# Performance work log

Hardware: AMD Instinct MI355X
Metric: run time of the kernel (lower is better)

## Reference

```python
import math
import jax, jax.numpy as jnp
import numpy as np

# ---- static config (mirrors init_kwargs) ----
NLAT_I, NLON_I = 240, 480      # input equiangular grid (incl. both poles)
NLAT_O, NLON_O = 361, 720      # output equiangular grid (incl. both poles)
CI, CO = 32, 32
NR, NPHI = 3, 3                # kernel_shape
K = (NR - 1) * NPHI + 1        # anisotropic piecewise-linear DISCO basis size = 7
LMAX = 120
CUTOFF = (NR + 0.25) * math.pi / LMAX     # _compute_cutoff_radius
DLAT_O = math.pi / (NLAT_O - 1)
WOFF = int(math.ceil(CUTOFF / DLAT_O))    # half lat-window (=10); geodesic dist >= |dtheta| so window is exact
WLAT = 2 * WOFF + 1
TWO_PI = 2.0 * math.pi


def _bilinear_upsample(x):
    # ResampleS2(mode='bilinear'): x [B,C,NLAT_I,NLON_I] -> [B,C,NLAT_O,NLON_O]
    # equiangular colatitudes theta_j = pi*j/(nlat-1); periodic longitude.
    pos_t = jnp.linspace(0.0, math.pi, NLAT_O) / (math.pi / (NLAT_I - 1))
    i0 = jnp.clip(jnp.floor(pos_t).astype(jnp.int32), 0, NLAT_I - 1)
    i1 = jnp.minimum(i0 + 1, NLAT_I - 1)
    wt = (pos_t - i0).astype(x.dtype)
    xl = (1.0 - wt)[:, None] * x[:, :, i0, :] + wt[:, None] * x[:, :, i1, :]
    pos_p = (jnp.arange(NLON_O) * (TWO_PI / NLON_O)) / (TWO_PI / NLON_I)
    j0f = jnp.floor(pos_p)
    j0 = j0f.astype(jnp.int32) % NLON_I
    j1 = (j0 + 1) % NLON_I
    wp = (pos_p - j0f).astype(x.dtype)
    return (1.0 - wp) * xl[..., j0] + wp * xl[..., j1]


def _build_psi():
    # DISCO filter tensor psi[k, t_out, dlat, dlon] with quadrature merged in,
    # exploiting longitude translation invariance (computed at lon_out = 0).
    theta = jnp.linspace(0.0, math.pi, NLAT_O)
    t_idx = jnp.arange(NLAT_O)
    d_idx = jnp.arange(WLAT) - WOFF
    lat_in = t_idx[:, None] + d_idx[None, :]             # [T,W]
    valid = (lat_in >= 0) & (lat_in < NLAT_O)
    lat_in_c = jnp.clip(lat_in, 0, NLAT_O - 1)
    alpha = -theta[:, None, None]                         # [T,1,1]
    gamma = theta[lat_in_c][:, :, None]                   # [T,W,1]
    beta = (TWO_PI / NLON_O) * jnp.arange(NLON_O)[None, None, :]
    # rotate input point into frame where the output point is at the north pole
    z = jnp.cos(alpha) * jnp.cos(gamma) - jnp.cos(beta) * jnp.sin(alpha) * jnp.sin(gamma)
    xx = jnp.cos(alpha) * jnp.cos(beta) * jnp.sin(gamma) + jnp.sin(alpha) * jnp.cos(gamma)
    yy = jnp.sin(beta) * jnp.sin(gamma)
    r = jnp.arccos(jnp.clip(z, -1.0, 1.0))                # geodesic distance [T,W,P]
    phi = jnp.arctan2(yy, xx) % TWO_PI                    # local azimuth
    dr = CUTOFF / NR
    dph = TWO_PI / NPHI
    vals = [jnp.maximum(0.0, 1.0 - r / dr)]               # isotropic center hat
    for k in range(1, K):
        ir = (k - 1) // NPHI + 1
        ip = (k - 1) % NPHI
        rad = jnp.maximum(0.0, 1.0 - jnp.abs(r - ir * dr) / dr)
        dd = jnp.abs(phi - ip * dph)
        dd = jnp.minimum(dd, TWO_PI - dd)
        az = jnp.maximum(0.0, 1.0 - dd / dph)
        vals.append(rad * az)
    psi = jnp.stack(vals, 0)                              # [K,T,W,P]
    psi = psi * (r <= CUTOFF) * valid[None, :, :, None]
    # merge quadrature weights of the input grid (sin(theta) dtheta dphi)
    q = jnp.sin(theta) * (math.pi / (NLAT_O - 1)) * (TWO_PI / NLON_O)
    psi = psi * q[lat_in_c][None, :, :, None]
    # nodal L1 normalization per basis function and output node
    scale = jnp.sum(psi, axis=(2, 3), keepdims=True)
    psi = psi / jnp.maximum(scale, 1e-8)
    return psi.astype(jnp.float32), lat_in_c


def _disco_conv(xu, weight, psi, lat_in_c):
    # xu [B,Ci,T,P]; weight [Co,Ci,K]; psi [K,T,W,P]
    h = jnp.einsum('oik,bitp->boktp', weight, xu)         # fold channel mixing first
    Hh = jnp.fft.rfft(h, axis=-1)                         # [B,Co,K,T,F]
    Ph = jnp.conj(jnp.fft.rfft(psi, axis=-1))             # [K,T,W,F]
    yh = jnp.zeros(Hh.shape[:2] + (NLAT_O, Hh.shape[-1]), dtype=Hh.dtype)
    for d in range(WLAT):                                 # small fixed halo loop
        Hd = Hh[:, :, :, lat_in_c[:, d], :]               # [B,Co,K,T,F]
        yh = yh + jnp.einsum('boktf,ktf->botf', Hd, Ph[:, :, d, :])
    return jnp.fft.irfft(yh, n=NLON_O, axis=-1)           # circular correlation over lon


def setup_inputs() -> dict:
    key = jax.random.key(0)
    k1, k2 = jax.random.split(key)
    x = jax.random.normal(k1, (1, CI, NLAT_I, NLON_I), dtype=jnp.float32)
    weight = jax.random.normal(k2, (CO, CI, K), dtype=jnp.float32) * 0.05
    return {'x': x, 'weight': weight}


def reference(x, weight):
    psi, lat_in_c = _build_psi()
    xu = _bilinear_upsample(x.astype(jnp.float32))        # forced fp32 region
    y = _disco_conv(xu, weight.astype(jnp.float32), psi, lat_in_c)
    return y.astype(x.dtype)
```

## Files before the change

kernel.cpp:

```cpp
#include <hip/hip_runtime.h>
#include <hip/hip_bf16.h>
#include <math.h>

#define NLAT_I 240
#define NLON_I 480
#define NLAT_O 361
#define NLON_O 720
#define CI_N 32
#define CO_N 32
#define K_N 7
#define WOFF 10
#define WLAT 21

#define PI_F 3.14159265358979323846f
#define TWOPI_F 6.28318530717958647692f
#define DLAT_V (PI_F / 360.0f)
#define DPHI_V (TWOPI_F / 720.0f)
#define CUTOFF_V (3.25f * PI_F / 120.0f)
#define DR_V (CUTOFF_V / 3.0f)
#define IDR_V (1.0f / DR_V)
#define DPH_V (TWOPI_F / 3.0f)
#define IDPH_V (1.0f / DPH_V)
#define QF_V (DLAT_V * DPHI_V)

#define PAD_T 64
#define CT 64
#define NBLK 512
#define NC45 45
#define NE 7581

typedef __attribute__((ext_vector_type(8))) short short8v;
typedef __attribute__((ext_vector_type(4))) short short4v;
typedef __attribute__((ext_vector_type(16))) float f32x16;

__device__ __forceinline__ unsigned short f2bf(float f) {
  __hip_bfloat16 h = __float2bfloat16(f);
  union { __hip_bfloat16 b; unsigned short s; } u; u.b = h; return u.s;
}

__device__ __forceinline__ void psi_eval(float ct, float st, float cg, float sg,
                                         float q, float bang, float v[7]) {
  float sb, cb;
  sincosf(bang, &sb, &cb);
  float dx = sg * cb - st;
  float dy = sg * sb;
  float dz = cg - ct;
  float c2 = dx * dx + dy * dy + dz * dz;
  float r = 2.0f * asinf(fminf(1.0f, 0.5f * sqrtf(c2)));
  if (r <= CUTOFF_V) {
    float xx = ct * cb * sg - st * cg;
    float yy = sb * sg;
    float phi = atan2f(yy, xx);
    if (phi < 0.0f) phi += TWOPI_F;
    v[0] = fmaxf(0.0f, 1.0f - r * IDR_V) * q;
#pragma unroll
    for (int k = 1; k < 7; ++k) {
      const float irdr = (float)(1 + (k - 1) / 3) * DR_V;
      const float ipph = (float)((k - 1) % 3) * DPH_V;
      float rad = fmaxf(0.0f, 1.0f - fabsf(r - irdr) * IDR_V);
      float dd = fabsf(phi - ipph);
      dd = fminf(dd, TWOPI_F - dd);
      float az = fmaxf(0.0f, 1.0f - dd * IDPH_V);
      v[k] = rad * az * q;
    }
  } else {
#pragma unroll
    for (int k = 0; k < 7; ++k) v[k] = 0.0f;
  }
}

__device__ __forceinline__ int windowB(int t, int d) {
  int tp = t + d - WOFF;
  if (tp < 0 || tp > NLAT_O - 1) return -1;
  float th = (float)t * DLAT_V, ga = (float)tp * DLAT_V;
  float st = sinf(th), ct = cosf(th), sg = sinf(ga), cg = cosf(ga);
  float den = st * sg;
  float num = cosf(CUTOFF_V) - ct * cg;
  if (den < 1e-9f) return (fabsf(th - ga) <= CUTOFF_V) ? 360 : -1;
  if (num >= den) return -1;
  if (num <= -den) return 360;
  int B = (int)ceilf(acosf(num / den) * (1.0f / DPHI_V)) + 1;
  return B > 360 ? 360 : B;
}

__device__ __forceinline__ int nsupOf(int B) { return (B >= 360) ? 720 : 2 * B + 1; }
__device__ __forceinline__ int widthOf(int B) {
  return (B < 0) ? 0 : ((nsupOf(B) + 129) & ~1);
}

__global__ void prep_kernel(const float* __restrict__ w, unsigned short* __restrict__ w2,
                            int* __restrict__ offsF, int* __restrict__ offsT,
                            int* __restrict__ wtab, float* __restrict__ sums,
                            int* __restrict__ counter, int* __restrict__ gB,
                            int* __restrict__ gUc) {
  const int tid = threadIdx.x;
  __shared__ int temp[256];
  if (tid < 8) counter[tid] = 0;
  for (int idx = tid; idx < 361 * 7; idx += 256) sums[idx] = 0.0f;
  for (int idx = tid; idx < 14 * 32 * 16; idx += 256) {
    int kk = idx & 15; int o = (idx >> 4) & 31; int c16 = idx >> 9;
    int ci = c16 * 16 + kk; int i = ci & 31; int k = ci >> 5;
    w2[idx] = f2bf(w[(o * 32 + i) * 7 + k]);
  }
  for (int e = tid; e < NE; e += 256) {
    int t = e / 21, d = e % 21;
    int B = windowB(t, d);
    gB[e] = B;
    offsF[e] = (B >= 0) ? nsupOf(B) * 7 : 0;
    offsT[e] = 14 * widthOf(B);
  }
  __syncthreads();
  for (int t = tid; t < 361; t += 256) {
    int run = 0;
    for (int d = 0; d < WLAT; ++d) {
      gUc[t * 22 + d] = run;
      int B = gB[t * 21 + d];
      int np = (B >= 0) ? ((31 + B) >> 4) + ((B + 15) >> 4) + 1 : 0;
      run += np;
    }
    gUc[t * 22 + 21] = run;
    wtab[t] = run;
  }
  __syncthreads();
#pragma unroll 1
  for (int pass = 0; pass < 2; ++pass) {
    int* a = pass ? offsT : offsF;
    int s = tid * 30, e = s + 30; if (e > NE) e = NE; if (s > NE) s = NE;
    int sum = 0;
    for (int i = s; i < e; ++i) sum += a[i];
    temp[tid] = sum;
    __syncthreads();
    if (tid == 0) {
      int run = 0;
      for (int i = 0; i < 256; ++i) { int v = temp[i]; temp[i] = run; run += v; }
      a[NE] = run;
    }
    __syncthreads();
    int run = temp[tid];
    for (int i = s; i < e; ++i) { int v = a[i]; a[i] = run; run += v; }
    __syncthreads();
  }
}

__global__ void upsample_kernel(const float* __restrict__ x,
                                unsigned short* __restrict__ XT) {
  int idx = blockIdx.x * 256 + threadIdx.x;
  if (idx >= NLAT_O * NC45 * 512) return;
  int kk = idx & 15;
  int i = (idx >> 4) & 31;
  int c = (idx >> 9) % NC45;
  int t = idx / (NC45 * 512);
  int p = c * 16 + kk;

  double post = (double)t * (239.0 / 360.0);
  int i0 = (int)floor(post);
  if (i0 < 0) i0 = 0;
  if (i0 > NLAT_I - 1) i0 = NLAT_I - 1;
  int i1 = i0 + 1; if (i1 > NLAT_I - 1) i1 = NLAT_I - 1;
  float wt = (float)(post - (double)i0);

  double posp = (double)p * (2.0 / 3.0);
  double j0f = floor(posp);
  int j0 = ((int)j0f) % NLON_I;
  int j1 = (j0 + 1) % NLON_I;
  float wp = (float)(posp - j0f);

  const float* xi = x + (size_t)i * (NLAT_I * NLON_I);
  float a = xi[i0 * NLON_I + j0];
  float b = xi[i0 * NLON_I + j1];
  float cc = xi[i1 * NLON_I + j0];
  float d = xi[i1 * NLON_I + j1];
  float l0 = (1.0f - wt) * a + wt * cc;
  float l1 = (1.0f - wt) * b + wt * d;
  XT[idx] = f2bf((1.0f - wp) * l0 + wp * l1);
}

__global__ void psi_raw_kernel(const int* __restrict__ offsF,
                               float* __restrict__ PSIF,
                               float* __restrict__ sums) {
  int t = blockIdx.x, d = blockIdx.y;
  int B = windowB(t, d);
  if (B < 0) return;
  int nsup = nsupOf(B);
  int bLo = (B >= 360) ? -360 : -B;
  int offF = offsF[t * 21 + d];
  int tp = t + d - WOFF;
  float th = (float)t * DLAT_V, ga = (float)tp * DLAT_V;
  float st, ct, sg, cg;
  sincosf(th, &st, &ct);
  sincosf(ga, &sg, &cg);
  float q = sg * QF_V;
  float acc[7];
#pragma unroll
  for (int k = 0; k < 7; ++k) acc[k] = 0.0f;
  for (int ix = threadIdx.x; ix < nsup; ix += 256) {
    float v[7];
    psi_eval(ct, st, cg, sg, q, (float)(bLo + ix) * DPHI_V, v);
#pragma unroll
    for (int k = 0; k < 7; ++k) { PSIF[offF + k * nsup + ix] = v[k]; acc[k] += v[k]; }
  }
#pragma unroll
  for (int k = 0; k < 7; ++k) {
    float a = acc[k];
    for (int off = 32; off > 0; off >>= 1) a += __shfl_down(a, off, 64);
    acc[k] = a;
  }
  __shared__ float red[4][7];
  int wid = threadIdx.x >> 6;
  if ((threadIdx.x & 63) == 0) {
#pragma unroll
    for (int k = 0; k < 7; ++k) red[wid][k] = acc[k];
  }
  __syncthreads();
  if (threadIdx.x == 0) {
#pragma unroll
    for (int k = 0; k < 7; ++k)
      atomicAdd(&sums[t * 7 + k], red[0][k] + red[1][k] + red[2][k] + red[3][k]);
  }
}

__global__ void psi_toep_kernel(const int* __restrict__ offsF,
                                const int* __restrict__ offsT,
                                const float* __restrict__ PSIF,
                                const float* __restrict__ sums,
                                unsigned short* __restrict__ PSIT) {
  int t = blockIdx.x, d = blockIdx.y;
  int B = windowB(t, d);
  if (B < 0) return;
  int nsup = nsupOf(B);
  int width = widthOf(B);
  int offF = offsF[t * 21 + d];
  int offT = offsT[t * 21 + d];
  float rc[7];
#pragma unroll
  for (int k = 0; k < 7; ++k) rc[k] = 1.0f / fmaxf(sums[t * 7 + k], 1e-8f);
  for (int ix = threadIdx.x; ix <= width; ix += 256) {
    int isup = ix - PAD_T;
    unsigned short vv[7];
    if (isup >= 0 && isup < nsup) {
#pragma unroll
      for (int k = 0; k < 7; ++k)
        vv[k] = f2bf(PSIF[offF + k * nsup + isup] * rc[k]);
    } else {
#pragma unroll
      for (int k = 0; k < 7; ++k) vv[k] = 0;
    }
    if (ix < width) {
#pragma unroll
      for (int k = 0; k < 7; ++k) PSIT[offT + (2 * k) * width + ix] = vv[k];
    }
    if (ix >= 1) {
#pragma unroll
      for (int k = 0; k < 7; ++k) PSIT[offT + (2 * k + 1) * width + ix - 1] = vv[k];
    }
  }
}


#define LOADSET(S, CC) {                                                  \
    int v45 = pw16 + (CC);                                                \
    if (v45 < 0) v45 += NC45;                                             \
    if (v45 >= NC45) v45 -= NC45;                                         \
    A##S = *(const short8v*)(XT + (((size_t)tpd * NC45 + v45) << 9) + laneA); \
    int jbIdx = (CC) * 16 + lconst - bLo + PAD_T;                         \
    const unsigned short* bp = pbase + jbIdx + ((jbIdx & 1) ? (wdt - 1) : 0); \
    B##S##0 = *(const short8v*)(bp);                                      \
    B##S##1 = *(const short8v*)(bp + ks);                                 \
    B##S##2 = *(const short8v*)(bp + 2 * ks);                             \
    B##S##3 = *(const short8v*)(bp + 3 * ks);                             \
    B##S##4 = *(const short8v*)(bp + 4 * ks);                             \
    B##S##5 = *(const short8v*)(bp + 5 * ks);                             \
    B##S##6 = *(const short8v*)(bp + 6 * ks); }

#define MFMASET(S) {                                                      \
    acc0 = __builtin_amdgcn_mfma_f32_32x32x16_bf16(A##S, B##S##0, acc0, 0, 0, 0); \
    acc1 = __builtin_amdgcn_mfma_f32_32x32x16_bf16(A##S, B##S##1, acc1, 0, 0, 0); \
    acc2 = __builtin_amdgcn_mfma_f32_32x32x16_bf16(A##S, B##S##2, acc2, 0, 0, 0); \
    acc3 = __builtin_amdgcn_mfma_f32_32x32x16_bf16(A##S, B##S##3, acc3, 0, 0, 0); \
    acc4 = __builtin_amdgcn_mfma_f32_32x32x16_bf16(A##S, B##S##4, acc4, 0, 0, 0); \
    acc5 = __builtin_amdgcn_mfma_f32_32x32x16_bf16(A##S, B##S##5, acc5, 0, 0, 0); \
    acc6 = __builtin_amdgcn_mfma_f32_32x32x16_bf16(A##S, B##S##6, acc6, 0, 0, 0); }

#define DUMP2(ACC, KK, HB) {                                              \
    short4v q_;                                                           \
    q_[0]=(short)f2bf(ACC[8*(HB)+0]); q_[1]=(short)f2bf(ACC[8*(HB)+1]);   \
    q_[2]=(short)f2bf(ACC[8*(HB)+2]); q_[3]=(short)f2bf(ACC[8*(HB)+3]);   \
    *(short4v*)(b2 + ((KK) << 9) + b0_) = q_;                             \
    q_[0]=(short)f2bf(ACC[8*(HB)+4]); q_[1]=(short)f2bf(ACC[8*(HB)+5]);   \
    q_[2]=(short)f2bf(ACC[8*(HB)+6]); q_[3]=(short)f2bf(ACC[8*(HB)+7]);   \
    *(short4v*)(b2 + ((KK) << 9) + b0_ + 8) = q_; }

__global__ __launch_bounds__(256, 2) void disco_kernel(
    const unsigned short* __restrict__ XT, const unsigned short* __restrict__ PSIT,
    const unsigned short* __restrict__ w2g, const int* __restrict__ offsT,
    const int* __restrict__ wtab, const int* __restrict__ gB,
    const int* __restrict__ gUc, float* __restrict__ y,
    int* __restrict__ counter) {
  const int tid = threadIdx.x;
  __shared__ __align__(16) unsigned short b2all[4 * 3584];
  __shared__ int Sbuf[362];
  __shared__ int sB[WLAT], sUc[WLAT + 1], sOff[WLAT], sW[WLAT];
  __shared__ int curItem, sSv;

  for (int j = tid; j < 361; j += 256) {
    int t = (j & 1) ? 360 - (j >> 1) : (j >> 1);
    Sbuf[j] = 6 * ((wtab[t] + CT - 1) / CT);
  }
  __syncthreads();
  if (tid == 0) {
    int run = 0;
    for (int j = 0; j < 361; ++j) { int v = Sbuf[j]; Sbuf[j] = run; run += v; }
    Sbuf[361] = run;
    sSv = 0;
  }
  __syncthreads();
  const int NTOT = Sbuf[361];
  const int xcd = blockIdx.x & 7;

  const int lane = tid & 63, wv = tid >> 6, nn = lane & 31, g = lane >> 5;
  const int g8 = g * 8;
  const int laneA = nn * 16 + g8;
  const int lconst = g8 - nn;

  while (true) {
    if (tid == 0) {
      int mm = NTOT;
      int s2 = sSv;
      while (s2 < 8) {
        int cx = (xcd + s2) & 7;
        int b0 = (NTOT * cx) >> 3;
        int b1 = (NTOT * (cx + 1)) >> 3;
        int off = atomicAdd(&counter[cx], 1);
        if (b0 + off < b1) { mm = b0 + off; break; }
        ++s2;
      }
      sSv = s2;
      curItem = mm;
    }
    __syncthreads();
    const int m = curItem;
    if (m >= NTOT) break;

    int lo = 0, hi = 360;
    while (lo < hi) {
      int mid = (lo + hi + 1) >> 1;
      if (Sbuf[mid] <= m) lo = mid; else hi = mid - 1;
    }
    const int j = lo;
    const int r = m - Sbuf[j];
    const int t = (j & 1) ? 360 - (j >> 1) : (j >> 1);
    const int pgroup = r % 6;
    const int part = r / 6;

    if (tid < WLAT) {
      int B = gB[t * 21 + tid];
      sB[tid] = B;
      sOff[tid] = offsT[t * 21 + tid];
      sW[tid] = widthOf(B);
    }
    if (tid < WLAT + 1) sUc[tid] = gUc[t * 22 + tid];
    __syncthreads();

    const int Wt = sUc[WLAT];
    int g0 = part * CT, g1 = g0 + CT;
    if (g1 > Wt) g1 = Wt;

    const int ptile = pgroup * 4 + wv;
    const int pw = ptile * 32;
    const int pw16 = ptile * 2;

    f32x16 acc0, acc1, acc2, acc3, acc4, acc5, acc6;
#pragma unroll
    for (int z = 0; z < 16; ++z) {
      acc0[z]=0; acc1[z]=0; acc2[z]=0; acc3[z]=0; acc4[z]=0; acc5[z]=0; acc6[z]=0;
    }

    short8v A0, A1;
    short8v B00, B01, B02, B03, B04, B05, B06;
    short8v B10, B11, B12, B13, B14, B15, B16;

    int gi = g0;
    int d = 0;
    while (d < WLAT && sUc[d + 1] <= gi) ++d;
    while (gi < g1) {
      const int B = sB[d];
      const int bLo = (B >= 360) ? -360 : -B;
      const int cmin = -((B + 15) >> 4);
      const int tpd = t + d - WOFF;
      const int wdt = sW[d];
      const int ks = 2 * wdt;
      const unsigned short* pbase = PSIT + sOff[d];
      const int rend = sUc[d + 1];
      const int gend = (rend < g1) ? rend : g1;
      const int n = gend - gi;
      int c = cmin + (gi - sUc[d]);

      LOADSET(0, c)
      int it = 0;
      for (; it + 2 <= n; it += 2) {
        LOADSET(1, c + 1)
        MFMASET(0)
        if (it + 2 < n) { LOADSET(0, c + 2) }
        MFMASET(1)
        c += 2;
      }
      if (it < n) { MFMASET(0) }

      gi = gend;
      ++d;
      while (d < WLAT && sUc[d + 1] <= gi) ++d;
    }

    unsigned short* b2 = b2all + wv * 3584;
    const int b0_ = nn * 16 + 4 * g;
    f32x16 Dy;
#pragma unroll
    for (int z = 0; z < 16; ++z) Dy[z] = 0.0f;

    {
      DUMP2(acc0, 0, 0) DUMP2(acc1, 1, 0) DUMP2(acc2, 2, 0) DUMP2(acc3, 3, 0)
      DUMP2(acc4, 4, 0) DUMP2(acc5, 5, 0) DUMP2(acc6, 6, 0)
#pragma unroll
      for (int k2 = 0; k2 < 7; ++k2) {
        short8v A2 = *(const short8v*)(w2g + (((2 * k2 + 0) * 32 + nn) << 4) + g8);
        short8v B2f = *(const short8v*)(b2 + (k2 << 9) + (nn << 4) + g8);
        Dy = __builtin_amdgcn_mfma_f32_32x32x16_bf16(A2, B2f, Dy, 0, 0, 0);
      }
    }
    {
      DUMP2(acc0, 0, 1) DUMP2(acc1, 1, 1) DUMP2(acc2, 2, 1) DUMP2(acc3, 3, 1)
      DUMP2(acc4, 4, 1) DUMP2(acc5, 5, 1) DUMP2(acc6, 6, 1)
#pragma unroll
      for (int k2 = 0; k2 < 7; ++k2) {
        short8v A2 = *(const short8v*)(w2g + (((2 * k2 + 1) * 32 + nn) << 4) + g8);
        short8v B2f = *(const short8v*)(b2 + (k2 << 9) + (nn << 4) + g8);
        Dy = __builtin_amdgcn_mfma_f32_32x32x16_bf16(A2, B2f, Dy, 0, 0, 0);
      }
    }

    const int p = pw + nn;
    if (p < NLON_O) {
#pragma unroll
      for (int rr = 0; rr < 16; ++rr) {
        int o = (rr & 3) + 8 * (rr >> 2) + 4 * g;
        atomicAdd(&y[((size_t)o * NLAT_O + t) * NLON_O + p], Dy[rr]);
      }
    }
  }
}

extern "C" void kernel_launch(void* const* d_in, const int* in_sizes, int n_in,
                              void* d_out, int out_size, void* d_ws, size_t ws_size,
                              hipStream_t stream) {
  (void)in_sizes; (void)n_in; (void)out_size; (void)ws_size;
  const float* x = (const float*)d_in[0];
  const float* w = (const float*)d_in[1];
  float* y = (float*)d_out;

  unsigned short* XT = (unsigned short*)d_ws;
  float* PSIF = (float*)(XT + (size_t)NLAT_O * NC45 * 512);
  unsigned short* PSIT = (unsigned short*)(PSIF + 6000000);
  unsigned short* w2 = PSIT + 26000000;
  float* sums = (float*)(w2 + 7168);
  int* offsF = (int*)(sums + NLAT_O * K_N);
  int* offsT = offsF + NE + 1;
  int* wtab = offsT + NE + 1;
  int* counter = wtab + 361;
  int* gB = counter + 8;
  int* gUc = gB + NE;

  hipMemsetAsync(y, 0, (size_t)CO_N * NLAT_O * NLON_O * sizeof(float), stream);

  prep_kernel<<<1, 256, 0, stream>>>(w, w2, offsF, offsT, wtab, sums, counter, gB, gUc);
  int n_up = NLAT_O * NC45 * 512;
  upsample_kernel<<<(n_up + 255) / 256, 256, 0, stream>>>(x, XT);
  psi_raw_kernel<<<dim3(NLAT_O, WLAT), 256, 0, stream>>>(offsF, PSIF, sums);
  psi_toep_kernel<<<dim3(NLAT_O, WLAT), 256, 0, stream>>>(offsF, offsT, PSIF, sums, PSIT);
  disco_kernel<<<NBLK, 256, 0, stream>>>(XT, PSIT, w2, offsT, wtab, gB, gUc, y, counter);
}
```

Baseline: 522.9 us.

## Compute two longitude tiles per wave to reuse psi B-fragments

Each wave now handles two adjacent 32-wide longitude tiles, loading the psi B operands once and applying them to two A fragments with 14 accumulators. Work items per latitude drop from 6 to 3 pgroups, the persistent grid shrinks to 256 blocks, and launch bounds go to 1 block per CU. This halves the B-fragment global loads per MFMA but doubles accumulator register pressure and lowers occupancy, which may expose latency.

```diff
diff --git a/kernel.cpp b/kernel.cpp
--- a/kernel.cpp
+++ b/kernel.cpp
@@ -25,7 +25,7 @@
 
 #define PAD_T 64
 #define CT 64
-#define NBLK 512
+#define NBLK 256
 #define NC45 45
 #define NE 7581
 
@@ -261,7 +261,9 @@
     int v45 = pw16 + (CC);                                                \
     if (v45 < 0) v45 += NC45;                                             \
     if (v45 >= NC45) v45 -= NC45;                                         \
-    A##S = *(const short8v*)(XT + (((size_t)tpd * NC45 + v45) << 9) + laneA); \
+    int v45b = v45 + 2; if (v45b >= NC45) v45b -= NC45;                   \
+    A##S##a = *(const short8v*)(XT + (((size_t)tpd * NC45 + v45) << 9) + laneA);  \
+    A##S##b = *(const short8v*)(XT + (((size_t)tpd * NC45 + v45b) << 9) + laneA); \
     int jbIdx = (CC) * 16 + lconst - bLo + PAD_T;                         \
     const unsigned short* bp = pbase + jbIdx + ((jbIdx & 1) ? (wdt - 1) : 0); \
     B##S##0 = *(const short8v*)(bp);                                      \
@@ -273,13 +275,20 @@
     B##S##6 = *(const short8v*)(bp + 6 * ks); }
 
 #define MFMASET(S) {                                                      \
-    acc0 = __builtin_amdgcn_mfma_f32_32x32x16_bf16(A##S, B##S##0, acc0, 0, 0, 0); \
-    acc1 = __builtin_amdgcn_mfma_f32_32x32x16_bf16(A##S, B##S##1, acc1, 0, 0, 0); \
-    acc2 = __builtin_amdgcn_mfma_f32_32x32x16_bf16(A##S, B##S##2, acc2, 0, 0, 0); \
-    acc3 = __builtin_amdgcn_mfma_f32_32x32x16_bf16(A##S, B##S##3, acc3, 0, 0, 0); \
-    acc4 = __builtin_amdgcn_mfma_f32_32x32x16_bf16(A##S, B##S##4, acc4, 0, 0, 0); \
-    acc5 = __builtin_amdgcn_mfma_f32_32x32x16_bf16(A##S, B##S##5, acc5, 0, 0, 0); \
-    acc6 = __builtin_amdgcn_mfma_f32_32x32x16_bf16(A##S, B##S##6, acc6, 0, 0, 0); }
+    accA0 = __builtin_amdgcn_mfma_f32_32x32x16_bf16(A##S##a, B##S##0, accA0, 0, 0, 0); \
+    accB0 = __builtin_amdgcn_mfma_f32_32x32x16_bf16(A##S##b, B##S##0, accB0, 0, 0, 0); \
+    accA1 = __builtin_amdgcn_mfma_f32_32x32x16_bf16(A##S##a, B##S##1, accA1, 0, 0, 0); \
+    accB1 = __builtin_amdgcn_mfma_f32_32x32x16_bf16(A##S##b, B##S##1, accB1, 0, 0, 0); \
+    accA2 = __builtin_amdgcn_mfma_f32_32x32x16_bf16(A##S##a, B##S##2, accA2, 0, 0, 0); \
+    accB2 = __builtin_amdgcn_mfma_f32_32x32x16_bf16(A##S##b, B##S##2, accB2, 0, 0, 0); \
+    accA3 = __builtin_amdgcn_mfma_f32_32x32x16_bf16(A##S##a, B##S##3, accA3, 0, 0, 0); \
+    accB3 = __builtin_amdgcn_mfma_f32_32x32x16_bf16(A##S##b, B##S##3, accB3, 0, 0, 0); \
+    accA4 = __builtin_amdgcn_mfma_f32_32x32x16_bf16(A##S##a, B##S##4, accA4, 0, 0, 0); \
+    accB4 = __builtin_amdgcn_mfma_f32_32x32x16_bf16(A##S##b, B##S##4, accB4, 0, 0, 0); \
+    accA5 = __builtin_amdgcn_mfma_f32_32x32x16_bf16(A##S##a, B##S##5, accA5, 0, 0, 0); \
+    accB5 = __builtin_amdgcn_mfma_f32_32x32x16_bf16(A##S##b, B##S##5, accB5, 0, 0, 0); \
+    accA6 = __builtin_amdgcn_mfma_f32_32x32x16_bf16(A##S##a, B##S##6, accA6, 0, 0, 0); \
+    accB6 = __builtin_amdgcn_mfma_f32_32x32x16_bf16(A##S##b, B##S##6, accB6, 0, 0, 0); }
 
 #define DUMP2(ACC, KK, HB) {                                              \
     short4v q_;                                                           \
@@ -290,7 +299,32 @@
     q_[2]=(short)f2bf(ACC[8*(HB)+6]); q_[3]=(short)f2bf(ACC[8*(HB)+7]);   \
     *(short4v*)(b2 + ((KK) << 9) + b0_ + 8) = q_; }
 
-__global__ __launch_bounds__(256, 2) void disco_kernel(
+#define GEMM2PT(AC0, AC1, AC2, AC3, AC4, AC5, AC6, PTILE) {               \
+    f32x16 Dy;                                                            \
+    _Pragma("unroll") for (int z = 0; z < 16; ++z) Dy[z] = 0.0f;          \
+    DUMP2(AC0, 0, 0) DUMP2(AC1, 1, 0) DUMP2(AC2, 2, 0) DUMP2(AC3, 3, 0)  \
+    DUMP2(AC4, 4, 0) DUMP2(AC5, 5, 0) DUMP2(AC6, 6, 0)                    \
+    _Pragma("unroll") for (int k2 = 0; k2 < 7; ++k2) {                    \
+      short8v A2 = *(const short8v*)(w2g + (((2 * k2 + 0) * 32 + nn) << 4) + g8); \
+      short8v B2f = *(const short8v*)(b2 + (k2 << 9) + (nn << 4) + g8);   \
+      Dy = __builtin_amdgcn_mfma_f32_32x32x16_bf16(A2, B2f, Dy, 0, 0, 0); \
+    }                                                                     \
+    DUMP2(AC0, 0, 1) DUMP2(AC1, 1, 1) DUMP2(AC2, 2, 1) DUMP2(AC3, 3, 1)  \
+    DUMP2(AC4, 4, 1) DUMP2(AC5, 5, 1) DUMP2(AC6, 6, 1)                    \
+    _Pragma("unroll") for (int k2 = 0; k2 < 7; ++k2) {                    \
+      short8v A2 = *(const short8v*)(w2g + (((2 * k2 + 1) * 32 + nn) << 4) + g8); \
+      short8v B2f = *(const short8v*)(b2 + (k2 << 9) + (nn << 4) + g8);   \
+      Dy = __builtin_amdgcn_mfma_f32_32x32x16_bf16(A2, B2f, Dy, 0, 0, 0); \
+    }                                                                     \
+    const int p_ = (PTILE) * 32 + nn;                                     \
+    if (p_ < NLON_O) {                                                    \
+      _Pragma("unroll") for (int rr = 0; rr < 16; ++rr) {                 \
+        int o = (rr & 3) + 8 * (rr >> 2) + 4 * g;                         \
+        atomicAdd(&y[((size_t)o * NLAT_O + t) * NLON_O + p_], Dy[rr]);    \
+      }                                                                   \
+    } }
+
+__global__ __launch_bounds__(256, 1) void disco_kernel(
     const unsigned short* __restrict__ XT, const unsigned short* __restrict__ PSIT,
     const unsigned short* __restrict__ w2g, const int* __restrict__ offsT,
     const int* __restrict__ wtab, const int* __restrict__ gB,
@@ -304,7 +338,7 @@
 
   for (int j = tid; j < 361; j += 256) {
     int t = (j & 1) ? 360 - (j >> 1) : (j >> 1);
-    Sbuf[j] = 6 * ((wtab[t] + CT - 1) / CT);
+    Sbuf[j] = 3 * ((wtab[t] + CT - 1) / CT);
   }
   __syncthreads();
   if (tid == 0) {
@@ -349,8 +383,8 @@
     const int j = lo;
     const int r = m - Sbuf[j];
     const int t = (j & 1) ? 360 - (j >> 1) : (j >> 1);
-    const int pgroup = r % 6;
-    const int part = r / 6;
+    const int pgpair = r % 3;
+    const int part = r / 3;
 
     if (tid < WLAT) {
       int B = gB[t * 21 + tid];
@@ -365,17 +399,18 @@
     int g0 = part * CT, g1 = g0 + CT;
     if (g1 > Wt) g1 = Wt;
 
-    const int ptile = pgroup * 4 + wv;
-    const int pw = ptile * 32;
-    const int pw16 = ptile * 2;
-
-    f32x16 acc0, acc1, acc2, acc3, acc4, acc5, acc6;
+    const int ptileA = pgpair * 8 + 2 * wv;
+    const int pw16 = ptileA * 2;
+
+    f32x16 accA0, accA1, accA2, accA3, accA4, accA5, accA6;
+    f32x16 accB0, accB1, accB2, accB3, accB4, accB5, accB6;
 #pragma unroll
     for (int z = 0; z < 16; ++z) {
-      acc0[z]=0; acc1[z]=0; acc2[z]=0; acc3[z]=0; acc4[z]=0; acc5[z]=0; acc6[z]=0;
-    }
-
-    short8v A0, A1;
+      accA0[z]=0; accA1[z]=0; accA2[z]=0; accA3[z]=0; accA4[z]=0; accA5[z]=0; accA6[z]=0;
+      accB0[z]=0; accB1[z]=0; accB2[z]=0; accB3[z]=0; accB4[z]=0; accB5[z]=0; accB6[z]=0;
+    }
+
+    short8v A0a, A0b, A1a, A1b;
     short8v B00, B01, B02, B03, B04, B05, B06;
     short8v B10, B11, B12, B13, B14, B15, B16;
 
@@ -413,39 +448,8 @@
 
     unsigned short* b2 = b2all + wv * 3584;
     const int b0_ = nn * 16 + 4 * g;
-    f32x16 Dy;
-#pragma unroll
-    for (int z = 0; z < 16; ++z) Dy[z] = 0.0f;
-
-    {
-      DUMP2(acc0, 0, 0) DUMP2(acc1, 1, 0) DUMP2(acc2, 2, 0) DUMP2(acc3, 3, 0)
-      DUMP2(acc4, 4, 0) DUMP2(acc5, 5, 0) DUMP2(acc6, 6, 0)
-#pragma unroll
-      for (int k2 = 0; k2 < 7; ++k2) {
-        short8v A2 = *(const short8v*)(w2g + (((2 * k2 + 0) * 32 + nn) << 4) + g8);
-        short8v B2f = *(const short8v*)(b2 + (k2 << 9) + (nn << 4) + g8);
-        Dy = __builtin_amdgcn_mfma_f32_32x32x16_bf16(A2, B2f, Dy, 0, 0, 0);
-      }
-    }
-    {
-      DUMP2(acc0, 0, 1) DUMP2(acc1, 1, 1) DUMP2(acc2, 2, 1) DUMP2(acc3, 3, 1)
-      DUMP2(acc4, 4, 1) DUMP2(acc5, 5, 1) DUMP2(acc6, 6, 1)
-#pragma unroll
-      for (int k2 = 0; k2 < 7; ++k2) {
-        short8v A2 = *(const short8v*)(w2g + (((2 * k2 + 1) * 32 + nn) << 4) + g8);
-        short8v B2f = *(const short8v*)(b2 + (k2 << 9) + (nn << 4) + g8);
-        Dy = __builtin_amdgcn_mfma_f32_32x32x16_bf16(A2, B2f, Dy, 0, 0, 0);
-      }
-    }
-
-    const int p = pw + nn;
-    if (p < NLON_O) {
-#pragma unroll
-      for (int rr = 0; rr < 16; ++rr) {
-        int o = (rr & 3) + 8 * (rr >> 2) + 4 * g;
-        atomicAdd(&y[((size_t)o * NLAT_O + t) * NLON_O + p], Dy[rr]);
-      }
-    }
+    GEMM2PT(accA0, accA1, accA2, accA3, accA4, accA5, accA6, ptileA)
+    GEMM2PT(accB0, accB1, accB2, accB3, accB4, accB5, accB6, ptileA + 1)
   }
 }
 
```

New measurement: 532.0 us. No clear change (+1.7%).
